# Kernel optimization log

Hardware: AMD Instinct MI355X
Metric: run time of the kernel (lower is better)

The kernel has to match this reference:

```python
import jax, jax.numpy as jnp
import numpy as np

LATENT_DIM = 512
ROWS = 262144


def setup_inputs() -> dict:
    key = jax.random.key(0)
    k_data, k_z = jax.random.split(key)
    data = jax.random.normal(k_data, (ROWS, LATENT_DIM), dtype=jnp.float32)
    # latentZ init: latentDimension * rand / sum(rand), shape (1, latentDimension)
    tz = jax.random.uniform(k_z, (1, LATENT_DIM), dtype=jnp.float32)
    latentZ = LATENT_DIM * tz / tz.sum()
    mu = jnp.zeros((1,), dtype=jnp.float32)
    tau = jnp.zeros((1,), dtype=jnp.float32)
    return {"data": data, "latentZ": latentZ, "mu": mu, "tau": tau}


def reference(data, latentZ, mu, tau):
    # Vectorized form of the per-row loop:
    # xz_i = latentZ * data[i]; irMu_i = (sum(xz_i)+mu)/(1+n)
    # irTau_i = (tau + n/2) / (1 + 0.5*sum((xz_i-mu)^2) + (irMu_i-mu)^2)
    n = data.shape[1]
    xz = data * latentZ                                  # (rows, n)
    s = jnp.sum(xz, axis=1, keepdims=True)               # (rows, 1)
    ir_mu = (s + mu) / (1.0 + n)                         # (rows, 1)
    sq = jnp.sum(jnp.square(xz - mu), axis=1, keepdims=True)  # (rows, 1)
    ir_tau = (tau + 0.5 * n) / (1.0 + 0.5 * sq + jnp.square(ir_mu - mu))
    return ir_mu, ir_tau
```

## Files before the change

### kernel.cpp

```cpp
#include <hip/hip_runtime.h>

#define ROWS 262144
#define LATENT 512

__global__ __launch_bounds__(256) void linear_svi_kernel(
    const float* __restrict__ data,
    const float* __restrict__ latentZ,
    const float* __restrict__ mu_p,
    const float* __restrict__ tau_p,
    float* __restrict__ out) {
  const int wave = threadIdx.x >> 6;
  const int lane = threadIdx.x & 63;
  const int row = (blockIdx.x << 2) + wave;

  const float mu = mu_p[0];
  const float tau = tau_p[0];

  const float4* zv = (const float4*)latentZ;
  const float4 z0 = zv[lane];
  const float4 z1 = zv[64 + lane];

  const float4* xv = (const float4*)(data + (size_t)row * LATENT);
  const float4 x0 = xv[lane];
  const float4 x1 = xv[64 + lane];

  float s = 0.0f;
  float sq = 0.0f;
  float p, d;
#define ACC(zz, xx)                 \
  p = (zz) * (xx);                  \
  s += p;                           \
  d = p - mu;                       \
  sq = fmaf(d, d, sq);
  ACC(z0.x, x0.x) ACC(z0.y, x0.y) ACC(z0.z, x0.z) ACC(z0.w, x0.w)
  ACC(z1.x, x1.x) ACC(z1.y, x1.y) ACC(z1.z, x1.z) ACC(z1.w, x1.w)
#undef ACC

  #pragma unroll
  for (int off = 32; off > 0; off >>= 1) {
    s += __shfl_xor(s, off, 64);
    sq += __shfl_xor(sq, off, 64);
  }

  if (lane == 0) {
    const float ir_mu = (s + mu) * (1.0f / (1.0f + (float)LATENT));
    const float dm = ir_mu - mu;
    const float ir_tau =
        (tau + 0.5f * (float)LATENT) / (1.0f + 0.5f * sq + dm * dm);
    out[row] = ir_mu;
    out[ROWS + row] = ir_tau;
  }
}

extern "C" void kernel_launch(void* const* d_in, const int* in_sizes, int n_in,
                              void* d_out, int out_size, void* d_ws, size_t ws_size,
                              hipStream_t stream) {
  const float* data    = (const float*)d_in[0];
  const float* latentZ = (const float*)d_in[1];
  const float* mu      = (const float*)d_in[2];
  const float* tau     = (const float*)d_in[3];
  float* out = (float*)d_out;

  dim3 grid(ROWS / 4);
  dim3 block(256);
  linear_svi_kernel<<<grid, block, 0, stream>>>(data, latentZ, mu, tau, out);
}
```

Measured before the change: 663.1 us.

## Use persistent grid-stride waves with register prefetch and nontemporal loads

Replaces the one-row-per-wave launch (65536 blocks) with 2048 persistent blocks whose waves each process 32 rows at a grid stride. The next row's data is prefetched into registers while the current row is reduced. Loads are marked nontemporal, and the two outputs are written by two lanes instead of one. The aim is to cut block launch overhead and hide memory latency on a bandwidth-bound streaming kernel, at the cost of fewer resident waves available to hide latency.

```diff
diff --git a/kernel.cpp b/kernel.cpp
--- a/kernel.cpp
+++ b/kernel.cpp
@@ -2,53 +2,70 @@
 
 #define ROWS 262144
 #define LATENT 512
+#define TPB 256
+#define BLOCKS 2048
+#define TOTAL_WAVES (BLOCKS * (TPB / 64))
+#define ROWS_PER_WAVE (ROWS / TOTAL_WAVES)
 
-__global__ __launch_bounds__(256) void linear_svi_kernel(
+typedef float vf4 __attribute__((ext_vector_type(4)));
+
+__global__ __launch_bounds__(TPB) void linear_svi_kernel(
     const float* __restrict__ data,
     const float* __restrict__ latentZ,
     const float* __restrict__ mu_p,
     const float* __restrict__ tau_p,
     float* __restrict__ out) {
-  const int wave = threadIdx.x >> 6;
   const int lane = threadIdx.x & 63;
-  const int row = (blockIdx.x << 2) + wave;
+  const int wave_g = (blockIdx.x << 2) + (threadIdx.x >> 6);
 
   const float mu = mu_p[0];
   const float tau = tau_p[0];
 
-  const float4* zv = (const float4*)latentZ;
-  const float4 z0 = zv[lane];
-  const float4 z1 = zv[64 + lane];
+  const vf4* zv = (const vf4*)latentZ;
+  const vf4 z0 = zv[lane];
+  const vf4 z1 = zv[64 + lane];
 
-  const float4* xv = (const float4*)(data + (size_t)row * LATENT);
-  const float4 x0 = xv[lane];
-  const float4 x1 = xv[64 + lane];
+  int row = wave_g;
+  const vf4* p = (const vf4*)(data + (size_t)row * LATENT);
+  vf4 x0 = __builtin_nontemporal_load(p + lane);
+  vf4 x1 = __builtin_nontemporal_load(p + 64 + lane);
 
-  float s = 0.0f;
-  float sq = 0.0f;
-  float p, d;
-#define ACC(zz, xx)                 \
-  p = (zz) * (xx);                  \
-  s += p;                           \
-  d = p - mu;                       \
-  sq = fmaf(d, d, sq);
-  ACC(z0.x, x0.x) ACC(z0.y, x0.y) ACC(z0.z, x0.z) ACC(z0.w, x0.w)
-  ACC(z1.x, x1.x) ACC(z1.y, x1.y) ACC(z1.z, x1.z) ACC(z1.w, x1.w)
+  for (int k = 0; k < ROWS_PER_WAVE; ++k) {
+    vf4 nx0, nx1;
+    const int nrow = row + TOTAL_WAVES;
+    if (k + 1 < ROWS_PER_WAVE) {
+      const vf4* np = (const vf4*)(data + (size_t)nrow * LATENT);
+      nx0 = __builtin_nontemporal_load(np + lane);
+      nx1 = __builtin_nontemporal_load(np + 64 + lane);
+    }
+
+    float s = 0.0f, sq = 0.0f, prod, dd;
+#define ACC(zz, xx)            \
+    prod = (zz) * (xx);        \
+    s += prod;                 \
+    dd = prod - mu;            \
+    sq = fmaf(dd, dd, sq);
+    ACC(z0.x, x0.x) ACC(z0.y, x0.y) ACC(z0.z, x0.z) ACC(z0.w, x0.w)
+    ACC(z1.x, x1.x) ACC(z1.y, x1.y) ACC(z1.z, x1.z) ACC(z1.w, x1.w)
 #undef ACC
 
-  #pragma unroll
-  for (int off = 32; off > 0; off >>= 1) {
-    s += __shfl_xor(s, off, 64);
-    sq += __shfl_xor(sq, off, 64);
-  }
+#pragma unroll
+    for (int off = 32; off > 0; off >>= 1) {
+      s += __shfl_xor(s, off, 64);
+      sq += __shfl_xor(sq, off, 64);
+    }
 
-  if (lane == 0) {
-    const float ir_mu = (s + mu) * (1.0f / (1.0f + (float)LATENT));
-    const float dm = ir_mu - mu;
-    const float ir_tau =
-        (tau + 0.5f * (float)LATENT) / (1.0f + 0.5f * sq + dm * dm);
-    out[row] = ir_mu;
-    out[ROWS + row] = ir_tau;
+    if (lane < 2) {
+      const float ir_mu = (s + mu) * (1.0f / 513.0f);
+      const float dm = ir_mu - mu;
+      const float ir_tau = (tau + 256.0f) / (1.0f + 0.5f * sq + dm * dm);
+      const float v = lane ? ir_tau : ir_mu;
+      out[(size_t)lane * ROWS + row] = v;
+    }
+
+    x0 = nx0;
+    x1 = nx1;
+    row = nrow;
   }
 }
 
@@ -61,7 +78,6 @@
   const float* tau     = (const float*)d_in[3];
   float* out = (float*)d_out;
 
-  dim3 grid(ROWS / 4);
-  dim3 block(256);
-  linear_svi_kernel<<<grid, block, 0, stream>>>(data, latentZ, mu, tau, out);
+  linear_svi_kernel<<<dim3(BLOCKS), dim3(TPB), 0, stream>>>(data, latentZ, mu,
+                                                            tau, out);
 }
```

Result: no change. 660.3 us (-0.4%).
